# Performance work log

Hardware: AMD Instinct MI355X
Metric: run time of the kernel (lower is better)

Reference implementation:

```python
import jax, jax.numpy as jnp
import numpy as np
import math

H = 16          # num heads
D = 64          # size_per_head
HID = H * D     # 1024
ROT = 32        # rotary_hsize <= D//2


def setup_inputs() -> dict:
    key = jax.random.key(0)
    ks = jax.random.split(key, 10)
    B, S = 2, 2048
    x = jax.random.normal(ks[0], (B, S, HID), dtype=jnp.float32)
    sinusoids = jax.random.normal(ks[1], (B, 2, S, ROT), dtype=jnp.float32)
    attention_bias = jnp.zeros((B, 1, S, S), dtype=jnp.float32)
    scale = 1.0 / math.sqrt(HID)
    Wq = jax.random.normal(ks[2], (HID, HID), dtype=jnp.float32) * scale
    bq = jnp.zeros((HID,), dtype=jnp.float32)
    Wk = jax.random.normal(ks[3], (HID, HID), dtype=jnp.float32) * scale
    bk = jnp.zeros((HID,), dtype=jnp.float32)
    Wv = jax.random.normal(ks[4], (HID, HID), dtype=jnp.float32) * scale
    bv = jnp.zeros((HID,), dtype=jnp.float32)
    Wo = jax.random.normal(ks[5], (HID, HID), dtype=jnp.float32) * scale
    return {"x": x, "sinusoids": sinusoids, "attention_bias": attention_bias,
            "Wq": Wq, "bq": bq, "Wk": Wk, "bk": bk, "Wv": Wv, "bv": bv, "Wo": Wo}


def _apply_rotary(qk, sin, cos):
    # qk: [B,S,H,D]; sin/cos: [B,S,1,ROT]
    r = qk[..., :ROT]
    # stack([-even, odd], -1).reshape -> interleaved (-x0, x1, -x2, x3, ...)
    rt = jnp.stack([-r[..., ::2], r[..., 1::2]], axis=-1).reshape(r.shape)
    return jnp.concatenate([r * cos + rt * sin, qk[..., ROT:]], axis=-1)


def reference(x, sinusoids, attention_bias, Wq, bq, Wk, bk, Wv, bv, Wo):
    B, S, _ = x.shape
    q = (x @ Wq + bq).reshape(B, S, H, D)
    k = (x @ Wk + bk).reshape(B, S, H, D)
    v = (x @ Wv + bv).reshape(B, S, H, D)
    sin = sinusoids[..., 0, :, None, :]  # [B,S,1,ROT]
    cos = sinusoids[..., 1, :, None, :]
    q = _apply_rotary(q, sin, cos)
    k = _apply_rotary(k, sin, cos)
    q = q / math.sqrt(D)
    scores = jnp.einsum('bqhd,bkhd->bhqk', q, k) + attention_bias
    probs = jax.nn.softmax(scores, axis=-1)
    out = jnp.einsum('bhqk,bkhd->bqhd', probs, v).reshape(B, S, HID)
    return out @ Wo
```

## Files before the change

### kernel.cpp

```cpp
#include <hip/hip_runtime.h>
#include <hip/hip_bf16.h>

#define H_   16
#define D_   64
#define HID  1024
#define S_   2048
#define B_   2
#define M_   (B_*S_)
#define ROT  32
#define LOG2E 1.44269504088896341f
#define QSCALE (0.125f * LOG2E)

typedef __bf16 bf16x8 __attribute__((ext_vector_type(8)));
typedef float  f32x4  __attribute__((ext_vector_type(4)));

#define XB_OFF   0u
#define WQT_OFF  (8u<<20)
#define WKT_OFF  (10u<<20)
#define WVT_OFF  (12u<<20)
#define WOT_OFF  (14u<<20)
#define F_OFF    (16u<<20)
#define QH_OFF   ((16u<<20) + (1u<<19))
#define KH_OFF   (QH_OFF + (8u<<20))
#define VT_OFF   (KH_OFF + (8u<<20))
#define AB_OFF   (VT_OFF + (8u<<20))

__device__ __forceinline__ float fexp2(float x) {
#if __has_builtin(__builtin_amdgcn_exp2f)
  return __builtin_amdgcn_exp2f(x);
#else
  return __expf(x * 0.69314718055994531f);
#endif
}

__device__ __forceinline__ unsigned pk2(float a, float b) {
  union { unsigned u; __bf16 h[2]; } w;
  w.h[0] = (__bf16)a; w.h[1] = (__bf16)b;
  return w.u;
}

__global__ __launch_bounds__(256) void prep_kernel(const float* __restrict__ x,
                                                   const float* __restrict__ sinu,
                                                   const float* __restrict__ abias,
                                                   const float* __restrict__ W0, const float* __restrict__ W1,
                                                   const float* __restrict__ W2, const float* __restrict__ W3,
                                                   __hip_bfloat16* __restrict__ xb,
                                                   float* __restrict__ F,
                                                   __hip_bfloat16* __restrict__ T0, __hip_bfloat16* __restrict__ T1,
                                                   __hip_bfloat16* __restrict__ T2, __hip_bfloat16* __restrict__ T3,
                                                   int* __restrict__ flag) {
  __shared__ float tile[32][33];
  int idx = blockIdx.x;
  int tid = threadIdx.x;
  if (idx < 4096) {
    int i = (idx * 256 + tid) * 4;
    float4 v = *(const float4*)(x + i);
    union { __hip_bfloat16 h[4]; uint2 u; } o;
    o.h[0] = __float2bfloat16(v.x);
    o.h[1] = __float2bfloat16(v.y);
    o.h[2] = __float2bfloat16(v.z);
    o.h[3] = __float2bfloat16(v.w);
    *(uint2*)(xb + i) = o.u;
  } else if (idx < 4608) {
    int i = (idx - 4096) * 256 + tid;
    int d  = i & (ROT-1);
    int bs = i >> 5;
    int s  = bs & (S_-1);
    int b  = bs >> 11;
    float sn = sinu[(((size_t)b*2 + 0)*S_ + s)*ROT + d];
    float cs = sinu[(((size_t)b*2 + 1)*S_ + s)*ROT + d];
    F[i] = cs + ((d & 1) ? sn : -sn);
  } else if (idx < 8704) {
    int widx = idx - 4608;
    int z    = widx >> 10;
    int rem  = widx & 1023;
    const float* W = (z==0) ? W0 : (z==1) ? W1 : (z==2) ? W2 : W3;
    __hip_bfloat16* T = (z==0) ? T0 : (z==1) ? T1 : (z==2) ? T2 : T3;
    int bx = (rem & 31) * 32;
    int by = (rem >> 5) * 32;
    int tx = tid & 31, ty = tid >> 5;
    #pragma unroll
    for (int i = 0; i < 4; i++)
      tile[ty + i*8][tx] = W[(size_t)(by + ty + i*8)*HID + bx + tx];
    __syncthreads();
    #pragma unroll
    for (int i = 0; i < 4; i++)
      T[(size_t)(bx + ty + i*8)*HID + by + tx] = __float2bfloat16(tile[tx][ty + i*8]);
  } else {
    size_t i = ((size_t)(idx - 8704) * 256 + tid) * 16;
    const uint4* p = (const uint4*)(abias + i);
    unsigned acc = 0;
    #pragma unroll
    for (int j = 0; j < 4; j++) {
      uint4 u = p[j];
      acc |= u.x | u.y | u.z | u.w;
    }
    if (acc) *flag = 1;
  }
}

__global__ __launch_bounds__(256) void qkv_kernel(const __hip_bfloat16* __restrict__ A,
                                                  const __hip_bfloat16* __restrict__ Bt,
                                                  const float* __restrict__ bq,
                                                  const float* __restrict__ bk,
                                                  const float* __restrict__ bv,
                                                  const float* __restrict__ F,
                                                  __hip_bfloat16* __restrict__ Qh,
                                                  __hip_bfloat16* __restrict__ Kh,
                                                  __hip_bfloat16* __restrict__ Vt) {
  __shared__ __align__(16) __bf16 Asm[2][128*32];
  __shared__ __align__(16) __bf16 Bsm[2][128*32];
  int tid  = threadIdx.x;
  int lane = tid & 63;
  int wv   = tid >> 6;
  int lr   = lane & 15;
  int qd   = lane >> 4;
  int row0 = blockIdx.y * 128;
  int col0 = blockIdx.x * 128;
  int wrow = (wv >> 1) * 64;
  int wcol = (wv & 1) * 64;

  int cg = ((tid & 3) ^ ((tid >> 2) & 3)) * 8;
  const __bf16* Ag = (const __bf16*)A  + (size_t)(row0 + (tid >> 2)) * HID + cg;
  const __bf16* Bg = (const __bf16*)Bt + (size_t)(col0 + (tid >> 2)) * HID + cg;

  f32x4 acc[4][4] = {};

  auto stage = [&](int buf, int k0) {
    __builtin_amdgcn_global_load_lds(Ag + k0,                  &Asm[buf][wv*512],        16, 0, 0);
    __builtin_amdgcn_global_load_lds(Ag + (size_t)64*HID + k0, &Asm[buf][2048 + wv*512], 16, 0, 0);
    __builtin_amdgcn_global_load_lds(Bg + k0,                  &Bsm[buf][wv*512],        16, 0, 0);
    __builtin_amdgcn_global_load_lds(Bg + (size_t)64*HID + k0, &Bsm[buf][2048 + wv*512], 16, 0, 0);
  };

  stage(0, 0);
  int buf = 0;
  for (int k0 = 0; k0 < HID; k0 += 32, buf ^= 1) {
    __syncthreads();
    if (k0 + 32 < HID) stage(buf ^ 1, k0 + 32);
    const __bf16* As = &Asm[buf][0];
    const __bf16* Bs = &Bsm[buf][0];
    bf16x8 a[4], b[4];
    #pragma unroll
    for (int i = 0; i < 4; i++) {
      int row = wrow + i*16 + lr;
      a[i] = *(const bf16x8*)(As + row*32 + ((qd ^ (row & 3)) * 8));
    }
    #pragma unroll
    for (int t = 0; t < 4; t++) {
      int row = wcol + t*16 + lr;
      b[t] = *(const bf16x8*)(Bs + row*32 + ((qd ^ (row & 3)) * 8));
    }
    #pragma unroll
    for (int i = 0; i < 4; i++)
      #pragma unroll
      for (int t = 0; t < 4; t++)
        acc[i][t] = __builtin_amdgcn_mfma_f32_16x16x32_bf16(a[i], b[t], acc[i][t], 0, 0, 0);
  }

  int proj = col0 >> 10;
  int nb   = (col0 & 1023) + wcol;
  const float* bias = (proj == 0) ? bq : ((proj == 1) ? bk : bv);
  #pragma unroll
  for (int i = 0; i < 4; i++) {
    #pragma unroll
    for (int t = 0; t < 4; t++) {
      int nl = nb + t*16 + lr;
      int h  = nl >> 6, d = nl & 63;
      if (proj == 2) {
        int m0 = row0 + wrow + i*16 + qd*4;
        int b2 = m0 >> 11, s0 = m0 & (S_-1);
        union { uint2 u; __bf16 hh[4]; } w;
        #pragma unroll
        for (int r = 0; r < 4; r++)
          w.hh[r] = (__bf16)(acc[i][t][r] + bias[nl]);
        int pos = (s0 & ~31) | ((s0 & 12) << 1) | ((s0 >> 2) & 4);
        *(uint2*)((__bf16*)Vt + ((size_t)(b2*H_ + h)*D_ + d)*S_ + pos) = w.u;
      } else {
        __hip_bfloat16* dst = (proj == 0) ? Qh : Kh;
        #pragma unroll
        for (int r = 0; r < 4; r++) {
          int m = row0 + wrow + i*16 + qd*4 + r;
          int b2 = m >> 11, s = m & (S_-1);
          float v = acc[i][t][r] + bias[nl];
          if (d < ROT) v *= F[(size_t)(b2*S_ + s)*ROT + d];
          if (proj == 0) v *= QSCALE;
          dst[((size_t)(b2*H_ + h)*S_ + s)*D_ + d] = __float2bfloat16(v);
        }
      }
    }
  }
}

__global__ __launch_bounds__(256) void gemm_o64(const __hip_bfloat16* __restrict__ A,
                                                const __hip_bfloat16* __restrict__ Bt,
                                                float* __restrict__ outf) {
  __shared__ __align__(16) __bf16 Asm[2][128*32];
  __shared__ __align__(16) __bf16 Bsm[2][64*32];
  int tid  = threadIdx.x;
  int lane = tid & 63;
  int wv   = tid >> 6;
  int lr   = lane & 15;
  int qd   = lane >> 4;
  int row0 = blockIdx.y * 128;
  int col0 = blockIdx.x * 64;
  int cg = ((tid & 3) ^ ((tid >> 2) & 3)) * 8;
  const __bf16* Ag = (const __bf16*)A  + (size_t)(row0 + (tid >> 2)) * HID + cg;
  const __bf16* Bg = (const __bf16*)Bt + (size_t)(col0 + (tid >> 2)) * HID + cg;

  f32x4 acc[2][4] = {};
  auto stage = [&](int buf, int k0) {
    __builtin_amdgcn_global_load_lds(Ag + k0,                  &Asm[buf][wv*512],        16, 0, 0);
    __builtin_amdgcn_global_load_lds(Ag + (size_t)64*HID + k0, &Asm[buf][2048 + wv*512], 16, 0, 0);
    __builtin_amdgcn_global_load_lds(Bg + k0,                  &Bsm[buf][wv*512],        16, 0, 0);
  };
  stage(0, 0);
  int buf = 0;
  for (int k0 = 0; k0 < HID; k0 += 32, buf ^= 1) {
    __syncthreads();
    if (k0 + 32 < HID) stage(buf ^ 1, k0 + 32);
    const __bf16* As = &Asm[buf][0];
    const __bf16* Bs = &Bsm[buf][0];
    bf16x8 a[2], b[4];
    #pragma unroll
    for (int i = 0; i < 2; i++) {
      int row = wv*32 + i*16 + lr;
      a[i] = *(const bf16x8*)(As + row*32 + ((qd ^ (row & 3)) * 8));
    }
    #pragma unroll
    for (int t = 0; t < 4; t++) {
      int row = t*16 + lr;
      b[t] = *(const bf16x8*)(Bs + row*32 + ((qd ^ (row & 3)) * 8));
    }
    #pragma unroll
    for (int i = 0; i < 2; i++)
      #pragma unroll
      for (int t = 0; t < 4; t++)
        acc[i][t] = __builtin_amdgcn_mfma_f32_16x16x32_bf16(a[i], b[t], acc[i][t], 0, 0, 0);
  }
  #pragma unroll
  for (int i = 0; i < 2; i++)
    #pragma unroll
    for (int t = 0; t < 4; t++)
      #pragma unroll
      for (int r = 0; r < 4; r++) {
        int m = row0 + wv*32 + i*16 + qd*4 + r;
        int n = col0 + t*16 + lr;
        outf[(size_t)m*HID + n] = acc[i][t][r];
      }
}

__global__ __launch_bounds__(256) void flash_kernel(const __hip_bfloat16* __restrict__ Qh,
                                                    const __hip_bfloat16* __restrict__ Kh,
                                                    const __hip_bfloat16* __restrict__ Vt,
                                                    const float* __restrict__ abias,
                                                    const int* __restrict__ flag,
                                                    __hip_bfloat16* __restrict__ Ab) {
  __shared__ __align__(16) __bf16 Ksm[2][64*64];
  __shared__ __align__(16) __bf16 Vsm[2][64*64];
  int tid  = threadIdx.x;
  int lane = tid & 63;
  int wv   = tid >> 6;
  int lr   = lane & 15;
  int qd   = lane >> 4;
  int idx  = blockIdx.x;
  int xcd  = idx & 7;
  int slot = idx >> 3;
  int bh   = xcd * 4 + (slot >> 4);
  int qblk = slot & 15;
  int b  = bh >> 4;
  int h  = bh & 15;
  int q0 = qblk * 128 + wv * 32;

  const __bf16* Kbase = (const __bf16*)Kh + (size_t)bh*S_*D_;
  const __bf16* Vbase = (const __bf16*)Vt + (size_t)bh*D_*S_;

  const __bf16* Qp = (const __bf16*)Qh + ((size_t)bh*S_ + q0 + lr)*D_ + qd*8;
  bf16x8 qa00 = *(const bf16x8*)(Qp);
  bf16x8 qa01 = *(const bf16x8*)(Qp + 32);
  bf16x8 qa10 = *(const bf16x8*)(Qp + 16*D_);
  bf16x8 qa11 = *(const bf16x8*)(Qp + 16*D_ + 32);

  int hasbias = *flag;
  const float* bp0 = abias + (size_t)b*S_*S_ + (size_t)(q0 + lr)*S_;
  const float* bp1 = bp0 + (size_t)16*S_;

  int rowb = tid >> 3;
  int cg8  = ((tid & 7) ^ (rowb & 7)) * 8;

  auto stageKV = [&](int bf, int kt2) {
    __builtin_amdgcn_global_load_lds(Kbase + (size_t)(kt2 + rowb)*D_ + cg8,      &Ksm[bf][wv*512],        16, 0, 0);
    __builtin_amdgcn_global_load_lds(Kbase + (size_t)(kt2 + 32 + rowb)*D_ + cg8, &Ksm[bf][2048 + wv*512], 16, 0, 0);
    __builtin_amdgcn_global_load_lds(Vbase + (size_t)rowb*S_ + kt2 + cg8,        &Vsm[bf][wv*512],        16, 0, 0);
    __builtin_amdgcn_global_load_lds(Vbase + (size_t)(32 + rowb)*S_ + kt2 + cg8, &Vsm[bf][2048 + wv*512], 16, 0, 0);
  };

  f32x4 oacc0[4] = {}, oacc1[4] = {};
  f32x4 lacc0 = {}, lacc1 = {};
  int sw = lr & 7;

  union { bf16x8 v; unsigned u[4]; } von;
  von.u[0] = von.u[1] = von.u[2] = von.u[3] = 0x3F803F80u;

  union Pu { bf16x8 v; unsigned u[4]; };
  Pu pb00 = {}, pb01 = {}, pb10 = {}, pb11 = {};
  bf16x8 vp0[4], vp1[4];

  stageKV(0, 0);
  int buf = 0;
  for (int kt = 0; kt < S_; kt += 64, buf ^= 1) {
    __syncthreads();
    if (kt + 64 < S_) stageKV(buf ^ 1, kt + 64);

    bf16x8 kf0[4], kf1[4];
    #pragma unroll
    for (int c = 0; c < 4; c++) {
      const __bf16* Kr = &Ksm[buf][(c*16 + lr)*64];
      kf0[c] = *(const bf16x8*)(Kr + ((qd       ^ sw) * 8));
      kf1[c] = *(const bf16x8*)(Kr + (((4 + qd) ^ sw) * 8));
    }

    if (kt > 0) {
      __builtin_amdgcn_s_setprio(1);
      #pragma unroll
      for (int t = 0; t < 4; t++) {
        oacc0[t] = __builtin_amdgcn_mfma_f32_16x16x32_bf16(vp0[t], pb00.v, oacc0[t], 0, 0, 0);
        oacc0[t] = __builtin_amdgcn_mfma_f32_16x16x32_bf16(vp1[t], pb01.v, oacc0[t], 0, 0, 0);
        oacc1[t] = __builtin_amdgcn_mfma_f32_16x16x32_bf16(vp0[t], pb10.v, oacc1[t], 0, 0, 0);
        oacc1[t] = __builtin_amdgcn_mfma_f32_16x16x32_bf16(vp1[t], pb11.v, oacc1[t], 0, 0, 0);
      }
      __builtin_amdgcn_s_setprio(0);
    }

    f32x4 s0[4], s1[4];
    __builtin_amdgcn_s_setprio(1);
    #pragma unroll
    for (int c = 0; c < 4; c++) {
      f32x4 z = {};
      z     = __builtin_amdgcn_mfma_f32_16x16x32_bf16(kf0[c], qa00, z, 0, 0, 0);
      s0[c] = __builtin_amdgcn_mfma_f32_16x16x32_bf16(kf1[c], qa01, z, 0, 0, 0);
      f32x4 z2 = {};
      z2    = __builtin_amdgcn_mfma_f32_16x16x32_bf16(kf0[c], qa10, z2, 0, 0, 0);
      s1[c] = __builtin_amdgcn_mfma_f32_16x16x32_bf16(kf1[c], qa11, z2, 0, 0, 0);
    }
    __builtin_amdgcn_s_setprio(0);

    if (hasbias) {
      #pragma unroll
      for (int c = 0; c < 4; c++) {
        float4 b0 = *(const float4*)(bp0 + kt + c*16 + qd*4);
        float4 b1 = *(const float4*)(bp1 + kt + c*16 + qd*4);
        s0[c][0] += b0.x*LOG2E; s0[c][1] += b0.y*LOG2E; s0[c][2] += b0.z*LOG2E; s0[c][3] += b0.w*LOG2E;
        s1[c][0] += b1.x*LOG2E; s1[c][1] += b1.y*LOG2E; s1[c][2] += b1.z*LOG2E; s1[c][3] += b1.w*LOG2E;
      }
    }

    #pragma unroll
    for (int c = 0; c < 2; c++) {
      pb00.u[2*c]   = pk2(fexp2(s0[c][0]), fexp2(s0[c][1]));
      pb00.u[2*c+1] = pk2(fexp2(s0[c][2]), fexp2(s0[c][3]));
      pb10.u[2*c]   = pk2(fexp2(s1[c][0]), fexp2(s1[c][1]));
      pb10.u[2*c+1] = pk2(fexp2(s1[c][2]), fexp2(s1[c][3]));
    }
    #pragma unroll
    for (int c = 2; c < 4; c++) {
      pb01.u[2*(c-2)]   = pk2(fexp2(s0[c][0]), fexp2(s0[c][1]));
      pb01.u[2*(c-2)+1] = pk2(fexp2(s0[c][2]), fexp2(s0[c][3]));
      pb11.u[2*(c-2)]   = pk2(fexp2(s1[c][0]), fexp2(s1[c][1]));
      pb11.u[2*(c-2)+1] = pk2(fexp2(s1[c][2]), fexp2(s1[c][3]));
    }

    lacc0 = __builtin_amdgcn_mfma_f32_16x16x32_bf16(von.v, pb00.v, lacc0, 0, 0, 0);
    lacc0 = __builtin_amdgcn_mfma_f32_16x16x32_bf16(von.v, pb01.v, lacc0, 0, 0, 0);
    lacc1 = __builtin_amdgcn_mfma_f32_16x16x32_bf16(von.v, pb10.v, lacc1, 0, 0, 0);
    lacc1 = __builtin_amdgcn_mfma_f32_16x16x32_bf16(von.v, pb11.v, lacc1, 0, 0, 0);

    #pragma unroll
    for (int t = 0; t < 4; t++) {
      const __bf16* Vr = &Vsm[buf][(t*16 + lr)*64];
      vp0[t] = *(const bf16x8*)(Vr + ((qd       ^ sw) * 8));
      vp1[t] = *(const bf16x8*)(Vr + (((4 + qd) ^ sw) * 8));
    }
  }

  __builtin_amdgcn_s_setprio(1);
  #pragma unroll
  for (int t = 0; t < 4; t++) {
    oacc0[t] = __builtin_amdgcn_mfma_f32_16x16x32_bf16(vp0[t], pb00.v, oacc0[t], 0, 0, 0);
    oacc0[t] = __builtin_amdgcn_mfma_f32_16x16x32_bf16(vp1[t], pb01.v, oacc0[t], 0, 0, 0);
    oacc1[t] = __builtin_amdgcn_mfma_f32_16x16x32_bf16(vp0[t], pb10.v, oacc1[t], 0, 0, 0);
    oacc1[t] = __builtin_amdgcn_mfma_f32_16x16x32_bf16(vp1[t], pb11.v, oacc1[t], 0, 0, 0);
  }
  __builtin_amdgcn_s_setprio(0);

  float inv0 = 1.0f / lacc0[0];
  float inv1 = 1.0f / lacc1[0];
  size_t ro0 = ((size_t)(b*S_ + q0 + lr))*HID + h*D_;
  size_t ro1 = ((size_t)(b*S_ + q0 + 16 + lr))*HID + h*D_;
  #pragma unroll
  for (int t = 0; t < 4; t++) {
    union { uint2 u; __bf16 hh[4]; } w0, w1;
    #pragma unroll
    for (int r = 0; r < 4; r++) {
      w0.hh[r] = (__bf16)(oacc0[t][r]*inv0);
      w1.hh[r] = (__bf16)(oacc1[t][r]*inv1);
    }
    *(uint2*)((__bf16*)Ab + ro0 + t*16 + qd*4) = w0.u;
    *(uint2*)((__bf16*)Ab + ro1 + t*16 + qd*4) = w1.u;
  }
}

extern "C" void kernel_launch(void* const* d_in, const int* in_sizes, int n_in,
                              void* d_out, int out_size, void* d_ws, size_t ws_size,
                              hipStream_t stream) {
  (void)in_sizes; (void)n_in; (void)out_size; (void)ws_size;
  const float* x     = (const float*)d_in[0];
  const float* sinu  = (const float*)d_in[1];
  const float* abias = (const float*)d_in[2];
  const float* Wq    = (const float*)d_in[3];
  const float* bq    = (const float*)d_in[4];
  const float* Wk    = (const float*)d_in[5];
  const float* bk    = (const float*)d_in[6];
  const float* Wv    = (const float*)d_in[7];
  const float* bv    = (const float*)d_in[8];
  const float* Wo    = (const float*)d_in[9];

  char* ws = (char*)d_ws;
  __hip_bfloat16* Xb  = (__hip_bfloat16*)(ws + XB_OFF);
  __hip_bfloat16* Wqt = (__hip_bfloat16*)(ws + WQT_OFF);
  __hip_bfloat16* Wkt = (__hip_bfloat16*)(ws + WKT_OFF);
  __hip_bfloat16* Wvt = (__hip_bfloat16*)(ws + WVT_OFF);
  __hip_bfloat16* Wot = (__hip_bfloat16*)(ws + WOT_OFF);
  float*          F   = (float*)(ws + F_OFF);
  __hip_bfloat16* Qh  = (__hip_bfloat16*)(ws + QH_OFF);
  __hip_bfloat16* Kh  = (__hip_bfloat16*)(ws + KH_OFF);
  __hip_bfloat16* Vt  = (__hip_bfloat16*)(ws + VT_OFF);
  __hip_bfloat16* Ab  = (__hip_bfloat16*)(ws + AB_OFF);
  int* flag = (int*)d_out;

  hipMemsetAsync(flag, 0, 4, stream);
  prep_kernel<<<10752, 256, 0, stream>>>(x, sinu, abias, Wq, Wk, Wv, Wo,
                                         Xb, F, Wqt, Wkt, Wvt, Wot, flag);

  qkv_kernel<<<dim3(3*HID/128, M_/128), 256, 0, stream>>>(
      Xb, Wqt, bq, bk, bv, F, Qh, Kh, Vt);

  flash_kernel<<<dim3(512), 256, 0, stream>>>(Qh, Kh, Vt, abias, flag, Ab);

  gemm_o64<<<dim3(HID/64, M_/128), 256, 0, stream>>>(Ab, Wot, (float*)d_out);
}
```

Baseline: 217.0 us.

## Load K/V fragments directly from global memory instead of LDS staging

Drops the double-buffered LDS staging of K and V tiles, which used global_load_lds and a per-iteration __syncthreads. Each wave now reads its K and V MFMA fragments straight from global memory into registers, and the V fragments are issued earlier in the iteration. This removes the barriers and the LDS round trip. In exchange, the four waves in a block each fetch the same K/V data, which multiplies L1/L2 traffic, and the loads are now 16-byte per-lane accesses strided across rows, exposing global latency that the prefetch previously hid.

```diff
diff --git a/kernel.cpp b/kernel.cpp
--- a/kernel.cpp
+++ b/kernel.cpp
@@ -256,8 +256,6 @@
                                                     const float* __restrict__ abias,
                                                     const int* __restrict__ flag,
                                                     __hip_bfloat16* __restrict__ Ab) {
-  __shared__ __align__(16) __bf16 Ksm[2][64*64];
-  __shared__ __align__(16) __bf16 Vsm[2][64*64];
   int tid  = threadIdx.x;
   int lane = tid & 63;
   int wv   = tid >> 6;
@@ -285,19 +283,8 @@
   const float* bp0 = abias + (size_t)b*S_*S_ + (size_t)(q0 + lr)*S_;
   const float* bp1 = bp0 + (size_t)16*S_;
 
-  int rowb = tid >> 3;
-  int cg8  = ((tid & 7) ^ (rowb & 7)) * 8;
-
-  auto stageKV = [&](int bf, int kt2) {
-    __builtin_amdgcn_global_load_lds(Kbase + (size_t)(kt2 + rowb)*D_ + cg8,      &Ksm[bf][wv*512],        16, 0, 0);
-    __builtin_amdgcn_global_load_lds(Kbase + (size_t)(kt2 + 32 + rowb)*D_ + cg8, &Ksm[bf][2048 + wv*512], 16, 0, 0);
-    __builtin_amdgcn_global_load_lds(Vbase + (size_t)rowb*S_ + kt2 + cg8,        &Vsm[bf][wv*512],        16, 0, 0);
-    __builtin_amdgcn_global_load_lds(Vbase + (size_t)(32 + rowb)*S_ + kt2 + cg8, &Vsm[bf][2048 + wv*512], 16, 0, 0);
-  };
-
   f32x4 oacc0[4] = {}, oacc1[4] = {};
   f32x4 lacc0 = {}, lacc1 = {};
-  int sw = lr & 7;
 
   union { bf16x8 v; unsigned u[4]; } von;
   von.u[0] = von.u[1] = von.u[2] = von.u[3] = 0x3F803F80u;
@@ -306,18 +293,16 @@
   Pu pb00 = {}, pb01 = {}, pb10 = {}, pb11 = {};
   bf16x8 vp0[4], vp1[4];
 
-  stageKV(0, 0);
-  int buf = 0;
-  for (int kt = 0; kt < S_; kt += 64, buf ^= 1) {
-    __syncthreads();
-    if (kt + 64 < S_) stageKV(buf ^ 1, kt + 64);
-
+  const __bf16* Kl = Kbase + (size_t)lr*D_ + qd*8;
+  const __bf16* Vl = Vbase + (size_t)lr*S_ + qd*8;
+
+  for (int kt = 0; kt < S_; kt += 64) {
     bf16x8 kf0[4], kf1[4];
     #pragma unroll
     for (int c = 0; c < 4; c++) {
-      const __bf16* Kr = &Ksm[buf][(c*16 + lr)*64];
-      kf0[c] = *(const bf16x8*)(Kr + ((qd       ^ sw) * 8));
-      kf1[c] = *(const bf16x8*)(Kr + (((4 + qd) ^ sw) * 8));
+      const __bf16* Kr = Kl + (size_t)(kt + c*16)*D_;
+      kf0[c] = *(const bf16x8*)(Kr);
+      kf1[c] = *(const bf16x8*)(Kr + 32);
     }
 
     if (kt > 0) {
@@ -332,6 +317,13 @@
       __builtin_amdgcn_s_setprio(0);
     }
 
+    #pragma unroll
+    for (int t = 0; t < 4; t++) {
+      const __bf16* Vr = Vl + (size_t)(t*16)*S_ + kt;
+      vp0[t] = *(const bf16x8*)(Vr);
+      vp1[t] = *(const bf16x8*)(Vr + 32);
+    }
+
     f32x4 s0[4], s1[4];
     __builtin_amdgcn_s_setprio(1);
     #pragma unroll
@@ -374,13 +366,6 @@
     lacc0 = __builtin_amdgcn_mfma_f32_16x16x32_bf16(von.v, pb01.v, lacc0, 0, 0, 0);
     lacc1 = __builtin_amdgcn_mfma_f32_16x16x32_bf16(von.v, pb10.v, lacc1, 0, 0, 0);
     lacc1 = __builtin_amdgcn_mfma_f32_16x16x32_bf16(von.v, pb11.v, lacc1, 0, 0, 0);
-
-    #pragma unroll
-    for (int t = 0; t < 4; t++) {
-      const __bf16* Vr = &Vsm[buf][(t*16 + lr)*64];
-      vp0[t] = *(const bf16x8*)(Vr + ((qd       ^ sw) * 8));
-      vp1[t] = *(const bf16x8*)(Vr + (((4 + qd) ^ sw) * 8));
-    }
   }
 
   __builtin_amdgcn_s_setprio(1);
```

After: 290.3 us. 1.34x slower.
